# Optimization experiments

Measured on AMD Instinct MI355X. Metric: run time of the kernel, lower is better.

Reference implementation:

```python
import jax, jax.numpy as jnp
import numpy as np

B = 1024
P = 8
D = 2048
NUM_IDS = 64
MARGIN = 0.3
EPS = 1e-12


def setup_inputs() -> dict:
    key = jax.random.key(0)
    k1, k2, k3 = jax.random.split(key, 3)
    feats = jax.random.normal(k1, (B, P * D), dtype=jnp.float32)
    labels = jax.random.randint(k2, (B,), 0, NUM_IDS, dtype=jnp.int64)
    subs = jax.random.randint(k3, (B,), 0, 2, dtype=jnp.int64)
    return {"feats": feats, "labels": labels, "subs": subs}


def reference(feats, labels, subs):
    b = feats.shape[0]
    f = feats.reshape(b, -1, D)  # [B, P, D]
    dt = f.dtype

    # Per-sample class centers via a single segment-mean pass
    # (equivalent to the original per-sample boolean-mask mean loop).
    seg_sum = jax.ops.segment_sum(f, labels, num_segments=NUM_IDS)  # [NUM_IDS, P, D]
    counts = jax.ops.segment_sum(jnp.ones((b,), dt), labels, num_segments=NUM_IDS)
    centers_by_id = seg_sum / jnp.maximum(counts, 1.0)[:, None, None]
    centers = centers_by_id[labels]  # [B, P, D]

    # dist_ap[i] = sum_p ||f[i,p] - center[i,p]||
    d_ap = jnp.sqrt(jnp.clip(jnp.sum((f - centers) ** 2, axis=-1), EPS, None)).sum(-1)  # [B]
    dist_ap = d_ap[:, None] + d_ap[None, :]  # [B, B]

    # pairwise_distance: dist_aa[i,j] = sum_p ||f[i,p] - f[j,p]||, via gemm trick
    sq = jnp.sum(f * f, axis=-1)  # [B, P]
    inner = jnp.einsum('ipd,jpd->ijp', f, f)  # [B, B, P]
    d2 = sq[:, None, :] + sq[None, :, :] - 2.0 * inner
    dist_aa = jnp.sqrt(jnp.clip(d2, EPS, None)).sum(-1)  # [B, B]

    # masked margin loss over negative (different-label) pairs
    mask = labels[:, None] != labels[None, :]  # [B, B] bool
    vals = jnp.clip(dist_ap - dist_aa + MARGIN, 0.0, None)
    maskf = mask.astype(dt)
    loss = jnp.sum(vals * maskf) / jnp.sum(maskf)
    return loss
```

## Files before the change

### kernel.cpp

```cpp
#include <hip/hip_runtime.h>
#include <hip/hip_bf16.h>

#define B_ 1024
#define P_ 8
#define D_ 2048
#define FD_ (P_ * D_)
#define NID 64
#define MARGIN_ 0.3f
#define EPS_ 1e-12f

typedef unsigned short u16;
typedef float float4_t __attribute__((ext_vector_type(4)));

#define AS1 __attribute__((address_space(1)))
#define AS3 __attribute__((address_space(3)))

__device__ __forceinline__ float bf2f(unsigned v) {
    unsigned x = v << 16;
    float f;
    __builtin_memcpy(&f, &x, 4);
    return f;
}

static const size_t OFF_COUNTS = 0;
static const size_t OFF_OFFS   = 256;
static const size_t OFF_PERM   = 512;
static const size_t OFF_NEG    = 4608;
static const size_t OFF_POS    = 8168;
static const size_t OFF_TICKET = 8172;
static const size_t OFF_S      = 8192;
static const size_t OFF_SQ     = 40960;
static const size_t OFF_DAP    = 73728;
static const size_t OFF_FB     = 131072;
static const size_t OFF_PD     = OFF_FB + (size_t)B_ * FD_;

__global__ void k_prep(const float* __restrict__ feats, const int* __restrict__ labels,
                       unsigned char* __restrict__ fb, float* __restrict__ sq,
                       float* countsf, int* offs, int* perm, float* negcnt) {
    int tid = threadIdx.x;
    if (blockIdx.x < B_) {
        int i = blockIdx.x;
        int p = tid >> 6, lane = tid & 63;
        const float* frow = feats + (size_t)i * FD_ + p * D_;
        unsigned char* brow = fb + (size_t)p * B_ * D_ + (size_t)i * D_;
        float s2 = 0.f;
#pragma unroll
        for (int ch = 0; ch < 8; ch++) {
            int d = ch * 256 + lane * 4;
            float4 f = *(const float4*)(frow + d);
            int pk = __builtin_amdgcn_cvt_pk_fp8_f32(f.x, f.y, 0, false);
            pk = __builtin_amdgcn_cvt_pk_fp8_f32(f.z, f.w, pk, true);
            *(unsigned int*)(brow + d) = (unsigned int)pk;
            s2 += f.x * f.x + f.y * f.y + f.z * f.z + f.w * f.w;
        }
        for (int o = 32; o; o >>= 1) s2 += __shfl_down(s2, o, 64);
        if (lane == 0) sq[i * P_ + p] = s2;
    } else {
        __shared__ int h[NID], o[NID], cur[NID];
        if (tid < NID) h[tid] = 0;
        __syncthreads();
        for (int i = tid; i < B_; i += 512) atomicAdd(&h[labels[i]], 1);
        __syncthreads();
        if (tid == 0) {
            int acc = 0;
            long long ss = 0;
            for (int c = 0; c < NID; c++) {
                o[c] = acc;
                acc += h[c];
                ss += (long long)h[c] * h[c];
            }
            *negcnt = (float)((long long)B_ * B_ - ss);
        }
        __syncthreads();
        if (tid < NID) {
            countsf[tid] = (float)h[tid];
            offs[tid] = o[tid];
            cur[tid] = o[tid];
        }
        __syncthreads();
        for (int i = tid; i < B_; i += 512) {
            int pos = atomicAdd(&cur[labels[i]], 1);
            perm[pos] = i;
        }
    }
}

__global__ __launch_bounds__(512, 4) void k_pairs(const unsigned char* __restrict__ fb,
                                                  const float* __restrict__ sq,
                                                  const int* __restrict__ labels,
                                                  float* __restrict__ S,
                                                  u16* __restrict__ pd) {
    const int p  = blockIdx.x;
    const int j0 = blockIdx.y * 128;
    const int i0 = blockIdx.z * 128;
    __shared__ __align__(16) unsigned char smem[65536];
    __shared__ float sqAs[128], sqBs[128];
    __shared__ int labA[128], labB[128];
    const int tid = threadIdx.x;
    const int lane = tid & 63, wid = tid >> 6;
    const int s = wid & 3, h = wid >> 2;
    if (tid < 128) {
        sqAs[tid] = sq[(i0 + tid) * 8 + p];
        labA[tid] = labels[i0 + tid];
    } else if (tid < 256) {
        int t = tid - 128;
        sqBs[t] = sq[(j0 + t) * 8 + p];
        labB[t] = labels[j0 + t];
    }

    const int wi = (s >> 1) * 64, wj = (s & 1) * 64;
    const int lhi = lane >> 4, llo = lane & 15;
    const int sl = llo & 7;
    const int lr = lane >> 3;
    const int lc = (lane & 7) ^ lr;

    unsigned char* const As = smem + h * 16384;
    unsigned char* const Bs = smem + 32768 + h * 16384;

    const size_t plbase = (size_t)p * ((size_t)B_ * D_);
    const size_t colbase = (size_t)h * 1024 + (size_t)lc * 16;
    const unsigned char* gA[4];
    const unsigned char* gB[4];
    unsigned char* lA[4];
    unsigned char* lB[4];
#pragma unroll
    for (int inst = 0; inst < 4; inst++) {
        int r0 = s * 32 + inst * 8;
        gA[inst] = fb + plbase + (size_t)(i0 + r0 + lr) * D_ + colbase;
        gB[inst] = fb + plbase + (size_t)(j0 + r0 + lr) * D_ + colbase;
        lA[inst] = As + r0 * 128;
        lB[inst] = Bs + r0 * 128;
    }

    float4_t acc[4][4];
#pragma unroll
    for (int a = 0; a < 4; a++)
#pragma unroll
        for (int b = 0; b < 4; b++) acc[a][b] = (float4_t){0.f, 0.f, 0.f, 0.f};

    for (int kb = 0; kb < 8; kb++) {
        const int koff = kb * 128;
        __syncthreads();
#pragma unroll
        for (int inst = 0; inst < 4; inst++) {
            __builtin_amdgcn_global_load_lds((const AS1 void*)(gA[inst] + koff),
                                             (AS3 void*)lA[inst], 16, 0, 0);
            __builtin_amdgcn_global_load_lds((const AS1 void*)(gB[inst] + koff),
                                             (AS3 void*)lB[inst], 16, 0, 0);
        }
        __syncthreads();
#pragma unroll
        for (int ks = 0; ks < 4; ks++) {
            const int pcb = ((2 * ks + (lhi >> 1)) ^ sl) * 16 + (lhi & 1) * 8;
            long af[4], bf[4];
#pragma unroll
            for (int a = 0; a < 4; a++) {
                af[a] = *(const long*)(As + (wi + a * 16 + llo) * 128 + pcb);
                bf[a] = *(const long*)(Bs + (wj + a * 16 + llo) * 128 + pcb);
            }
#pragma unroll
            for (int a = 0; a < 4; a++)
#pragma unroll
                for (int b = 0; b < 4; b++)
                    acc[a][b] = __builtin_amdgcn_mfma_f32_16x16x32_fp8_fp8(
                        af[a], bf[b], acc[a][b], 0, 0, 0);
        }
    }
    __syncthreads();
    float* ep = (float*)smem;
    if (h == 1) {
#pragma unroll
        for (int a = 0; a < 4; a++)
#pragma unroll
            for (int b = 0; b < 4; b++)
                *(float4_t*)&ep[(((s * 4 + a) * 4 + b) * 64 + lane) * 4] = acc[a][b];
    }
    __syncthreads();
    if (h == 0) {
        u16* outp = pd + (size_t)p * B_ * B_;
        float rs[4][4];
#pragma unroll
        for (int a = 0; a < 4; a++)
#pragma unroll
            for (int r = 0; r < 4; r++) rs[a][r] = 0.f;
#pragma unroll
        for (int a = 0; a < 4; a++) {
            int la0 = labA[wi + a * 16 + lhi * 4 + 0];
            int la1 = labA[wi + a * 16 + lhi * 4 + 1];
            int la2 = labA[wi + a * 16 + lhi * 4 + 2];
            int la3 = labA[wi + a * 16 + lhi * 4 + 3];
#pragma unroll
            for (int b = 0; b < 4; b++) {
                float4_t o = *(const float4_t*)&ep[(((s * 4 + a) * 4 + b) * 64 + lane) * 4];
                int jl = wj + b * 16 + llo;
                int lb = labB[jl];
#pragma unroll
                for (int r = 0; r < 4; r++) {
                    int il = wi + a * 16 + lhi * 4 + r;
                    float t = acc[a][b][r] + o[r];
                    float d2 = sqAs[il] + sqBs[jl] - 2.0f * t;
                    outp[(size_t)(i0 + il) * B_ + (j0 + jl)] =
                        __bfloat16_as_ushort(__float2bfloat16(sqrtf(fmaxf(d2, EPS_))));
                    int la = (r == 0) ? la0 : (r == 1) ? la1 : (r == 2) ? la2 : la3;
                    if (lb == la) rs[a][r] += t;
                }
            }
        }
#pragma unroll
        for (int a = 0; a < 4; a++)
#pragma unroll
            for (int r = 0; r < 4; r++) {
                float v = rs[a][r];
                v += __shfl_xor(v, 1, 64);
                v += __shfl_xor(v, 2, 64);
                v += __shfl_xor(v, 4, 64);
                v += __shfl_xor(v, 8, 64);
                if (llo == 0)
                    atomicAdd(&S[(size_t)(i0 + wi + a * 16 + lhi * 4 + r) * 8 + p], v);
            }
    }
}

__global__ void k_dap(const float* __restrict__ S, const float* __restrict__ sq,
                      const float* __restrict__ countsf, const int* __restrict__ offs,
                      const int* __restrict__ perm, float* __restrict__ dap) {
    int c = blockIdx.x;
    int tid = threadIdx.x;
    int cnt = (int)countsf[c];
    int off = offs[c];
    __shared__ float T[8];
    if (tid < 8) {
        float t = 0.f;
        for (int m = 0; m < cnt; m++) t += S[(size_t)perm[off + m] * 8 + tid];
        T[tid] = t;
    }
    __syncthreads();
    float n = fmaxf((float)cnt, 1.f);
    float inv = 1.f / n, inv2 = inv * inv;
    for (int m = tid; m < cnt; m += 64) {
        int i = perm[off + m];
        float d = 0.f;
#pragma unroll
        for (int p = 0; p < 8; p++) {
            float d2 = sq[i * 8 + p] - 2.f * inv * S[(size_t)i * 8 + p] + inv2 * T[p];
            d += sqrtf(fmaxf(d2, EPS_));
        }
        dap[i] = d;
    }
}

__global__ void k_lossred(const u16* __restrict__ pd, const float* __restrict__ dap,
                          const int* __restrict__ labels, float* possum,
                          const float* negcnt, int* ticket, float* out) {
    int i = blockIdx.x;
    int tid = threadIdx.x;
    float di = dap[i];
    int li = labels[i];
    int jb = tid * 4;
    float daa0 = 0.f, daa1 = 0.f, daa2 = 0.f, daa3 = 0.f;
#pragma unroll
    for (int p = 0; p < 8; p++) {
        uint2 v = *(const uint2*)&pd[((size_t)p << 20) + (size_t)i * B_ + jb];
        daa0 += bf2f(v.x & 0xFFFFu);
        daa1 += bf2f(v.x >> 16);
        daa2 += bf2f(v.y & 0xFFFFu);
        daa3 += bf2f(v.y >> 16);
    }
    float lsum = 0.f;
    float daas[4] = {daa0, daa1, daa2, daa3};
#pragma unroll
    for (int q = 0; q < 4; q++) {
        int j = jb + q;
        if (labels[j] != li) lsum += fmaxf(di + dap[j] - daas[q] + MARGIN_, 0.f);
    }
    for (int o = 32; o; o >>= 1) lsum += __shfl_down(lsum, o, 64);
    __shared__ float red[4];
    int wid = tid >> 6, lane = tid & 63;
    if (lane == 0) red[wid] = lsum;
    __syncthreads();
    if (tid == 0) {
        atomicAdd(possum, red[0] + red[1] + red[2] + red[3]);
        __threadfence();
        int t = atomicAdd(ticket, 1);
        if (t == B_ - 1) {
            float total = atomicAdd(possum, 0.0f);
            out[0] = total / negcnt[0];
        }
    }
}

extern "C" void kernel_launch(void* const* d_in, const int* in_sizes, int n_in,
                              void* d_out, int out_size, void* d_ws, size_t ws_size,
                              hipStream_t stream) {
    const float* feats = (const float*)d_in[0];
    const int* labels  = (const int*)d_in[1];
    float* out = (float*)d_out;

    char* w = (char*)d_ws;
    float* countsf = (float*)(w + OFF_COUNTS);
    int* offs      = (int*)(w + OFF_OFFS);
    int* perm      = (int*)(w + OFF_PERM);
    float* negcnt  = (float*)(w + OFF_NEG);
    float* possum  = (float*)(w + OFF_POS);
    int* ticket    = (int*)(w + OFF_TICKET);
    float* S       = (float*)(w + OFF_S);
    float* sq      = (float*)(w + OFF_SQ);
    float* dap     = (float*)(w + OFF_DAP);
    unsigned char* fb = (unsigned char*)(w + OFF_FB);
    u16* pd        = (u16*)(w + OFF_PD);

    hipMemsetAsync(w + OFF_POS, 0, (OFF_S - OFF_POS) + (size_t)B_ * P_ * 4, stream);

    k_prep<<<B_ + 1, 512, 0, stream>>>(feats, labels, fb, sq, countsf, offs, perm, negcnt);
    k_pairs<<<dim3(8, 8, 8), 512, 0, stream>>>(fb, sq, labels, S, pd);
    k_dap<<<NID, 64, 0, stream>>>(S, sq, countsf, offs, perm, dap);
    k_lossred<<<B_, 256, 0, stream>>>(pd, dap, labels, possum, negcnt, ticket, out);
}
```

Measured before the change: 181.9 us.

## Exploit pairwise symmetry: compute only upper-triangular tiles and half of loss pairs

The pairwise GEMM kernel now launches only the 36 upper-triangular 128x128 tile pairs per part instead of all 64, mapping a linear block index to (ti, tj). Off-diagonal tiles also add their same-label column sums into S, so the per-sample inner-product sums stay complete. The loss reduction now visits only j > i and doubles the sum, relying on the symmetry of dist_ap, dist_aa and the mask. In exchange, the loss kernel's reads become scalar 2-byte strided loads instead of vectorized ones, and its work is unbalanced across rows. The loss reads pd only at tile-level upper positions, but within diagonal tiles it needs j > i entries, which are written.

```diff
diff --git a/kernel.cpp b/kernel.cpp
--- a/kernel.cpp
+++ b/kernel.cpp
@@ -90,9 +90,11 @@
                                                   const int* __restrict__ labels,
                                                   float* __restrict__ S,
                                                   u16* __restrict__ pd) {
-    const int p  = blockIdx.x;
-    const int j0 = blockIdx.y * 128;
-    const int i0 = blockIdx.z * 128;
+    const int p = blockIdx.x;
+    int rem = blockIdx.y, ti = 0;
+    while (rem >= 8 - ti) { rem -= 8 - ti; ti++; }
+    const int tj = ti + rem;
+    const int i0 = ti * 128, j0 = tj * 128;
     __shared__ __align__(16) unsigned char smem[65536];
     __shared__ float sqAs[128], sqBs[128];
     __shared__ int labA[128], labB[128];
@@ -179,10 +181,13 @@
     if (h == 0) {
         u16* outp = pd + (size_t)p * B_ * B_;
         float rs[4][4];
+        float cs[4];
 #pragma unroll
         for (int a = 0; a < 4; a++)
 #pragma unroll
             for (int r = 0; r < 4; r++) rs[a][r] = 0.f;
+#pragma unroll
+        for (int b = 0; b < 4; b++) cs[b] = 0.f;
 #pragma unroll
         for (int a = 0; a < 4; a++) {
             int la0 = labA[wi + a * 16 + lhi * 4 + 0];
@@ -202,7 +207,10 @@
                     outp[(size_t)(i0 + il) * B_ + (j0 + jl)] =
                         __bfloat16_as_ushort(__float2bfloat16(sqrtf(fmaxf(d2, EPS_))));
                     int la = (r == 0) ? la0 : (r == 1) ? la1 : (r == 2) ? la2 : la3;
-                    if (lb == la) rs[a][r] += t;
+                    if (lb == la) {
+                        rs[a][r] += t;
+                        cs[b] += t;
+                    }
                 }
             }
         }
@@ -218,6 +226,16 @@
                 if (llo == 0)
                     atomicAdd(&S[(size_t)(i0 + wi + a * 16 + lhi * 4 + r) * 8 + p], v);
             }
+        if (tj > ti) {
+#pragma unroll
+            for (int b = 0; b < 4; b++) {
+                float v = cs[b];
+                v += __shfl_xor(v, 16, 64);
+                v += __shfl_xor(v, 32, 64);
+                if (lhi == 0)
+                    atomicAdd(&S[(size_t)(j0 + wj + b * 16 + llo) * 8 + p], v);
+            }
+        }
     }
 }
 
@@ -256,23 +274,17 @@
     int tid = threadIdx.x;
     float di = dap[i];
     int li = labels[i];
-    int jb = tid * 4;
-    float daa0 = 0.f, daa1 = 0.f, daa2 = 0.f, daa3 = 0.f;
-#pragma unroll
-    for (int p = 0; p < 8; p++) {
-        uint2 v = *(const uint2*)&pd[((size_t)p << 20) + (size_t)i * B_ + jb];
-        daa0 += bf2f(v.x & 0xFFFFu);
-        daa1 += bf2f(v.x >> 16);
-        daa2 += bf2f(v.y & 0xFFFFu);
-        daa3 += bf2f(v.y >> 16);
-    }
     float lsum = 0.f;
-    float daas[4] = {daa0, daa1, daa2, daa3};
-#pragma unroll
-    for (int q = 0; q < 4; q++) {
-        int j = jb + q;
-        if (labels[j] != li) lsum += fmaxf(di + dap[j] - daas[q] + MARGIN_, 0.f);
-    }
+    for (int j = i + 1 + tid; j < B_; j += 256) {
+        if (labels[j] != li) {
+            float daa = 0.f;
+#pragma unroll
+            for (int p = 0; p < 8; p++)
+                daa += bf2f(pd[((size_t)p << 20) + (size_t)i * B_ + j]);
+            lsum += fmaxf(di + dap[j] - daa + MARGIN_, 0.f);
+        }
+    }
+    lsum *= 2.0f;
     for (int o = 32; o; o >>= 1) lsum += __shfl_down(lsum, o, 64);
     __shared__ float red[4];
     int wid = tid >> 6, lane = tid & 63;
@@ -312,7 +324,7 @@
     hipMemsetAsync(w + OFF_POS, 0, (OFF_S - OFF_POS) + (size_t)B_ * P_ * 4, stream);
 
     k_prep<<<B_ + 1, 512, 0, stream>>>(feats, labels, fb, sq, countsf, offs, perm, negcnt);
-    k_pairs<<<dim3(8, 8, 8), 512, 0, stream>>>(fb, sq, labels, S, pd);
+    k_pairs<<<dim3(8, 36), 512, 0, stream>>>(fb, sq, labels, S, pd);
     k_dap<<<NID, 64, 0, stream>>>(S, sq, countsf, offs, perm, dap);
     k_lossred<<<B_, 256, 0, stream>>>(pd, dap, labels, possum, negcnt, ticket, out);
 }
```

Result: no change. 179.0 us (-1.6%).
